# Kernel tuning notes

Measured on AMD Instinct MI355X. Metric: run time of the kernel, lower is better.

Reference implementation:

```python
import jax, jax.numpy as jnp
import numpy as np

N_NODES = 50000
N_EDGES = 800000
IN_FEATS = 256
HIDDEN = 256
NUM_CLASSES = 64


def setup_inputs() -> dict:
    key = jax.random.key(0)
    k1, k2, k3, k4 = jax.random.split(key, 4)
    features = jax.random.normal(k1, (N_NODES, IN_FEATS), dtype=jnp.float32)
    edge_index = jax.random.randint(k2, (2, N_EDGES), 0, N_NODES, dtype=jnp.int32)
    W1 = jax.random.normal(k3, (IN_FEATS, HIDDEN), dtype=jnp.float32) * (1.0 / np.sqrt(IN_FEATS))
    b1 = jnp.zeros((HIDDEN,), dtype=jnp.float32)
    W2 = jax.random.normal(k4, (HIDDEN, NUM_CLASSES), dtype=jnp.float32) * (1.0 / np.sqrt(HIDDEN))
    b2 = jnp.zeros((NUM_CLASSES,), dtype=jnp.float32)
    return {"features": features, "edge_index": edge_index, "W1": W1, "b1": b1, "W2": W2, "b2": b2}


def reference(features, edge_index, W1, b1, W2, b2):
    # Two-layer GCN: h = A_hat @ relu(A_hat @ X W1 + b1) W2 + b2
    # A_hat uses symmetric degree normalization 1/sqrt(d_src * d_dst)
    N = features.shape[0]
    src, dst = edge_index[0], edge_index[1]
    ones = jnp.ones((src.shape[0],), dtype=features.dtype)
    deg_out = jax.ops.segment_sum(ones, src, num_segments=N)  # out-degree per node
    deg_in = jax.ops.segment_sum(ones, dst, num_segments=N)   # in-degree per node
    inv_sqrt_out = jax.lax.rsqrt(jnp.maximum(deg_out, 1.0))
    inv_sqrt_in = jax.lax.rsqrt(jnp.maximum(deg_in, 1.0))
    edge_norm = (inv_sqrt_out[src] * inv_sqrt_in[dst])[:, None]  # [E,1]

    def gcn_layer(x, W, b):
        h = x @ W                      # transform first (reduces message width)
        msg = h[src] * edge_norm       # [E, out]
        agg = jax.ops.segment_sum(msg, dst, num_segments=N)
        return agg + b

    h = jax.nn.relu(gcn_layer(features, W1, b1))
    return gcn_layer(h, W2, b2)
```

## Files before the change

### kernel.cpp

```cpp
#include <hip/hip_runtime.h>

#define NN 50000
#define MPAD 50048
#define NE 800000
#define SCAN_BLOCKS 49

typedef short short8 __attribute__((ext_vector_type(8)));
typedef float f32x4 __attribute__((ext_vector_type(4)));

__device__ __forceinline__ unsigned short f2bf(float x) {
    unsigned u = __builtin_bit_cast(unsigned, x);
    u += 0x7FFFu + ((u >> 16) & 1u);
    return (unsigned short)(u >> 16);
}
__device__ __forceinline__ float bf2f(unsigned short h) {
    unsigned u = ((unsigned)h) << 16;
    return __builtin_bit_cast(float, u);
}
__device__ __forceinline__ void gld16(const void* g, void* l) {
    __builtin_amdgcn_global_load_lds(
        (const __attribute__((address_space(1))) unsigned int*)g,
        (__attribute__((address_space(3))) unsigned int*)l, 16, 0, 0);
}


__global__ __launch_bounds__(256) void count_kernel(const int* __restrict__ src,
    const int* __restrict__ dst, int* __restrict__ cnt_out, int* __restrict__ cnt_in, int E)
{
    int e = blockIdx.x * 256 + threadIdx.x;
    if (e < E) {
        atomicAdd(&cnt_out[src[e]], 1);
        atomicAdd(&cnt_in[dst[e]], 1);
    }
}

__global__ __launch_bounds__(256) void inv_kernel(const int* __restrict__ cnt_out,
    const int* __restrict__ cnt_in, float* __restrict__ inv_out, float* __restrict__ inv_in, int n)
{
    int i = blockIdx.x * 256 + threadIdx.x;
    if (i < n) {
        inv_out[i] = rsqrtf(fmaxf((float)cnt_out[i], 1.0f));
        inv_in[i]  = rsqrtf(fmaxf((float)cnt_in[i], 1.0f));
    }
}

__global__ __launch_bounds__(256) void scanA_kernel(const int* __restrict__ cnt,
    int* __restrict__ bsum)
{
    __shared__ int sm[256];
    int b = blockIdx.x, tid = threadIdx.x;
    int base = b * 1024 + tid * 4;
    int s = 0;
    #pragma unroll
    for (int i = 0; i < 4; ++i) {
        int idx = base + i;
        if (idx < NN) s += cnt[idx];
    }
    sm[tid] = s;
    __syncthreads();
    for (int off = 128; off > 0; off >>= 1) {
        if (tid < off) sm[tid] += sm[tid + off];
        __syncthreads();
    }
    if (tid == 0) bsum[b] = sm[0];
}

__global__ __launch_bounds__(64) void scanB_kernel(const int* __restrict__ bsum,
    int* __restrict__ bexcl)
{
    int tid = threadIdx.x;
    int orig = (tid < SCAN_BLOCKS) ? bsum[tid] : 0;
    int v = orig;
    #pragma unroll
    for (int off = 1; off < 64; off <<= 1) {
        int u = __shfl_up(v, off, 64);
        if (tid >= off) v += u;
    }
    if (tid < SCAN_BLOCKS) bexcl[tid] = v - orig;
}

__global__ __launch_bounds__(256) void scanC_kernel(const int* __restrict__ cnt,
    const int* __restrict__ bexcl, int* __restrict__ rs)
{
    __shared__ int wsum[4];
    int b = blockIdx.x, tid = threadIdx.x;
    int lane = tid & 63, wv = tid >> 6;
    int base = b * 1024 + tid * 4;
    int v[4]; int s = 0;
    #pragma unroll
    for (int i = 0; i < 4; ++i) {
        int idx = base + i;
        v[i] = (idx < NN) ? cnt[idx] : 0;
        s += v[i];
    }
    int inc = s;
    #pragma unroll
    for (int off = 1; off < 64; off <<= 1) {
        int u = __shfl_up(inc, off, 64);
        if (lane >= off) inc += u;
    }
    if (lane == 63) wsum[wv] = inc;
    __syncthreads();
    int wo = 0;
    for (int i = 0; i < wv; ++i) wo += wsum[i];
    int run = wo + (inc - s) + bexcl[b];
    #pragma unroll
    for (int i = 0; i < 4; ++i) {
        int idx = base + i;
        if (idx < NN) { rs[idx] = run; run += v[i]; }
    }
}

__global__ __launch_bounds__(256) void fill_kernel(const int* __restrict__ src,
    const int* __restrict__ dst, int* __restrict__ rs, int* __restrict__ csr_src, int E)
{
    int e = blockIdx.x * 256 + threadIdx.x;
    if (e < E) {
        int slot = atomicAdd(&rs[dst[e]], 1);
        csr_src[slot] = src[e];
    }
}

__global__ __launch_bounds__(256) void splitX_kernel(const float* __restrict__ X,
    unsigned short* __restrict__ Xh, unsigned short* __restrict__ Xl)
{
    int i = blockIdx.x * 256 + threadIdx.x;
    if (i >= NN * 32) return;
    int r = i >> 5, c = i & 31;
    const float* src = X + (size_t)r * 256 + c * 8;
    float4 a0 = *(const float4*)src;
    float4 a1 = *(const float4*)(src + 4);
    float xs[8] = {a0.x, a0.y, a0.z, a0.w, a1.x, a1.y, a1.z, a1.w};
    short8 hv, lv;
    #pragma unroll
    for (int t = 0; t < 8; ++t) {
        unsigned short h = f2bf(xs[t]);
        hv[t] = (short)h;
        lv[t] = (short)f2bf(xs[t] - bf2f(h));
    }
    size_t off = (size_t)r * 256 + (c >> 3) * 64 + (((c & 7) ^ (r & 7)) * 8);
    *(short8*)&Xh[off] = hv;
    *(short8*)&Xl[off] = lv;
}

__global__ __launch_bounds__(256) void splitW_kernel(const float* __restrict__ W,
    unsigned short* __restrict__ BT, int N)
{
    int i = blockIdx.x * 256 + threadIdx.x;
    if (i >= N * 32) return;
    int col = i >> 5, kc = i & 31;
    short8 hv, lv;
    #pragma unroll
    for (int j = 0; j < 8; ++j) {
        float x = W[(size_t)(kc * 8 + j) * N + col];
        unsigned short h = f2bf(x);
        hv[j] = (short)h;
        lv[j] = (short)f2bf(x - bf2f(h));
    }
    size_t base = (size_t)col * 512;
    size_t o = (kc >> 3) * 64 + (((kc & 7) ^ (col & 7)) * 8);
    *(short8*)&BT[base + o] = hv;
    *(short8*)&BT[base + 256 + o] = lv;
}

template<int BN, bool SWZ_OUT>
__global__ __launch_bounds__(256) void gemm_sp_kernel(
    const unsigned short* __restrict__ Ah, const unsigned short* __restrict__ Al,
    const unsigned short* __restrict__ BT, const float* __restrict__ inv_out,
    unsigned short* __restrict__ C, int M, int Ntot)
{
    constexpr int WN = BN / 2;
    constexpr int NF = WN / 16;
    constexpr int BI = BN / 32;
    __shared__ unsigned short As[128 * 64];
    __shared__ unsigned short Bs[BN * 64];
    const int tid = threadIdx.x;
    const int w = tid >> 6, lane = tid & 63;
    const int wm = w >> 1, wn = w & 1;
    const int r = lane & 15, kg = lane >> 4;
    const int rowbase = blockIdx.x * 128;
    const int colbase = blockIdx.y * BN;

    f32x4 acc[4][NF] = {};

    for (int t = 0; t < 12; ++t) {
        const int ph = t >> 2;
        const int kb = t & 3;
        const unsigned short* Asrc = (ph == 1) ? Al : Ah;
        const int bsel = (ph == 2) ? 256 : 0;
        #pragma unroll
        for (int i = 0; i < 4; ++i) {
            int ct = (w * 4 + i) * 64 + lane;
            int row = ct >> 3, c = ct & 7;
            gld16(Asrc + (size_t)(rowbase + row) * 256 + kb * 64 + c * 8,
                  (unsigned short*)As + (size_t)ct * 8);
        }
        #pragma unroll
        for (int i = 0; i < BI; ++i) {
            int ct = (w * BI + i) * 64 + lane;
            int col = ct >> 3, c = ct & 7;
            gld16(BT + (size_t)(colbase + col) * 512 + bsel + kb * 64 + c * 8,
                  (unsigned short*)Bs + (size_t)ct * 8);
        }
        __syncthreads();
        #pragma unroll
        for (int ks = 0; ks < 2; ++ks) {
            short8 af[4];
            #pragma unroll
            for (int mf = 0; mf < 4; ++mf) {
                int row = wm * 64 + mf * 16 + r;
                af[mf] = *(const short8*)&As[row * 64 + (((ks * 4 + kg) ^ (row & 7)) * 8)];
            }
            #pragma unroll
            for (int nf = 0; nf < NF; ++nf) {
                int col = wn * WN + nf * 16 + r;
                short8 bf = *(const short8*)&Bs[col * 64 + (((ks * 4 + kg) ^ (col & 7)) * 8)];
                #pragma unroll
                for (int mf = 0; mf < 4; ++mf)
                    acc[mf][nf] = __builtin_amdgcn_mfma_f32_16x16x32_bf16(af[mf], bf, acc[mf][nf], 0, 0, 0);
            }
        }
        __syncthreads();
    }

    #pragma unroll
    for (int mf = 0; mf < 4; ++mf) {
        #pragma unroll
        for (int reg = 0; reg < 4; ++reg) {
            int orow = rowbase + wm * 64 + mf * 16 + kg * 4 + reg;
            if (orow >= M) continue;
            float sc = inv_out[orow];
            #pragma unroll
            for (int nf = 0; nf < NF; ++nf) {
                int ocol = colbase + wn * WN + nf * 16 + r;
                unsigned short v = f2bf(acc[mf][nf][reg] * sc);
                if (SWZ_OUT) {
                    size_t idx = (size_t)orow * 256 + (ocol >> 6) * 64
                               + ((((ocol >> 3) & 7) ^ (orow & 7)) * 8) + (ocol & 7);
                    C[idx] = v;
                } else {
                    C[(size_t)orow * Ntot + ocol] = v;
                }
            }
        }
    }
}

__global__ __launch_bounds__(256) void gather256_kernel(const unsigned short* __restrict__ t1s,
    const int* __restrict__ csr_src, const int* __restrict__ rs,
    const float* __restrict__ inv_in, const float* __restrict__ b1,
    unsigned short* __restrict__ Ah2, unsigned short* __restrict__ Al2)
{
    int n = (int)((blockIdx.x * 256 + threadIdx.x) >> 6);
    int lane = threadIdx.x & 63;
    if (n >= NN) return;
    int begin = (n == 0) ? 0 : rs[n - 1];
    int end = rs[n];
    int c = lane >> 1, h = lane & 1;
    int cc = c & 7;
    int sub = (c >> 3) * 64 + h * 4;
    float a0 = 0.f, a1 = 0.f, a2 = 0.f, a3 = 0.f;
    #pragma unroll 2
    for (int j = begin; j < end; ++j) {
        int s = csr_src[j];
        ushort4 v = *(const ushort4*)&t1s[(size_t)s * 256 + sub + ((cc ^ (s & 7)) * 8)];
        a0 += bf2f(v.x); a1 += bf2f(v.y); a2 += bf2f(v.z); a3 += bf2f(v.w);
    }
    float win = inv_in[n];
    int k0 = c * 8 + h * 4;
    float4 bb = *(const float4*)&b1[k0];
    float x0 = fmaxf(fmaf(a0, win, bb.x), 0.f);
    float x1 = fmaxf(fmaf(a1, win, bb.y), 0.f);
    float x2 = fmaxf(fmaf(a2, win, bb.z), 0.f);
    float x3 = fmaxf(fmaf(a3, win, bb.w), 0.f);
    unsigned short h0 = f2bf(x0), h1 = f2bf(x1), h2 = f2bf(x2), h3 = f2bf(x3);
    ushort4 hv = {h0, h1, h2, h3};
    ushort4 lv = {f2bf(x0 - bf2f(h0)), f2bf(x1 - bf2f(h1)),
                  f2bf(x2 - bf2f(h2)), f2bf(x3 - bf2f(h3))};
    size_t off = (size_t)n * 256 + sub + ((cc ^ (n & 7)) * 8);
    *(ushort4*)&Ah2[off] = hv;
    *(ushort4*)&Al2[off] = lv;
}

__global__ __launch_bounds__(256) void gather64_kernel(const unsigned short* __restrict__ t2,
    const int* __restrict__ csr_src, const int* __restrict__ rs,
    const float* __restrict__ inv_in, const float* __restrict__ b2,
    float* __restrict__ out)
{
    int n = (int)((blockIdx.x * 256 + threadIdx.x) >> 6);
    int lane = threadIdx.x & 63;
    if (n >= NN) return;
    int begin = (n == 0) ? 0 : rs[n - 1];
    int end = rs[n];
    float acc = 0.f;
    #pragma unroll 2
    for (int j = begin; j < end; ++j) {
        int s = csr_src[j];
        acc += bf2f(t2[(size_t)s * 64 + lane]);
    }
    out[(size_t)n * 64 + lane] = fmaf(acc, inv_in[n], b2[lane]);
}

extern "C" void kernel_launch(void* const* d_in, const int* in_sizes, int n_in,
                              void* d_out, int out_size, void* d_ws, size_t ws_size,
                              hipStream_t stream)
{
    const float* features = (const float*)d_in[0];
    const int*   edge_index = (const int*)d_in[1];
    const float* W1 = (const float*)d_in[2];
    const float* b1 = (const float*)d_in[3];
    const float* W2 = (const float*)d_in[4];
    const float* b2 = (const float*)d_in[5];
    float* out = (float*)d_out;
    const int* src = edge_index;
    const int* dst = edge_index + NE;

    char* p = (char*)d_ws;
    int* cnt_out = (int*)p;            p += (size_t)NN * 4;
    int* cnt_in  = (int*)p;            p += (size_t)NN * 4;
    float* inv_out = (float*)p;        p += (size_t)NN * 4;
    float* inv_in  = (float*)p;        p += (size_t)NN * 4;
    int* rs      = (int*)p;            p += (size_t)NN * 4;
    int* csr_src = (int*)p;            p += (size_t)NE * 4;
    int* bsum    = (int*)p;            p += 64 * 4;
    int* bexcl   = (int*)p;            p += 64 * 4;
    unsigned short* W1T = (unsigned short*)p;  p += (size_t)256 * 512 * 2;
    unsigned short* W2T = (unsigned short*)p;  p += (size_t)64 * 512 * 2;
    unsigned short* Xh  = (unsigned short*)p;  p += (size_t)MPAD * 256 * 2;
    unsigned short* Xl  = (unsigned short*)p;  p += (size_t)MPAD * 256 * 2;
    unsigned short* t1s = (unsigned short*)p;  p += (size_t)NN * 256 * 2;
    unsigned short* Ah2 = (unsigned short*)p;  p += (size_t)MPAD * 256 * 2;
    unsigned short* Al2 = (unsigned short*)p;  p += (size_t)MPAD * 256 * 2;
    unsigned short* t2  = (unsigned short*)p;  p += (size_t)NN * 64 * 2;

    hipMemsetAsync(cnt_out, 0, 2 * (size_t)NN * sizeof(int), stream);

    count_kernel<<<(NE + 255) / 256, 256, 0, stream>>>(src, dst, cnt_out, cnt_in, NE);
    inv_kernel<<<(NN + 255) / 256, 256, 0, stream>>>(cnt_out, cnt_in, inv_out, inv_in, NN);
    scanA_kernel<<<SCAN_BLOCKS, 256, 0, stream>>>(cnt_in, bsum);
    scanB_kernel<<<1, 64, 0, stream>>>(bsum, bexcl);
    scanC_kernel<<<SCAN_BLOCKS, 256, 0, stream>>>(cnt_in, bexcl, rs);
    fill_kernel<<<(NE + 255) / 256, 256, 0, stream>>>(src, dst, rs, csr_src, NE);

    splitX_kernel<<<(NN * 32 + 255) / 256, 256, 0, stream>>>(features, Xh, Xl);
    splitW_kernel<<<(256 * 32 + 255) / 256, 256, 0, stream>>>(W1, W1T, 256);
    splitW_kernel<<<(64 * 32 + 255) / 256, 256, 0, stream>>>(W2, W2T, 64);

    gemm_sp_kernel<128, true><<<dim3(MPAD / 128, 2), 256, 0, stream>>>(
        Xh, Xl, W1T, inv_out, t1s, NN, 256);

    gather256_kernel<<<(NN * 64 + 255) / 256, 256, 0, stream>>>(
        t1s, csr_src, rs, inv_in, b1, Ah2, Al2);

    gemm_sp_kernel<64, false><<<dim3(MPAD / 128, 1), 256, 0, stream>>>(
        Ah2, Al2, W2T, inv_out, t2, NN, 64);

    gather64_kernel<<<(NN * 64 + 255) / 256, 256, 0, stream>>>(
        t2, csr_src, rs, inv_in, b2, out);
}
```

Measured before the change: 343.0 us.

## Fuse split-bf16 GEMM phases into one K loop and unroll gather loops by four

The split-precision GEMM previously made three separate passes over K (hi*hi, lo*hi, hi*lo), reloading A and B tiles each time. It now loads the hi and lo tiles of A and B together and issues all three MFMAs per fragment in a single pass, which cuts the number of global-to-LDS loads and barriers. The cost is twice the LDS footprint and more registers per thread, which may lower occupancy. The two gather kernels are also manually unrolled by four so more independent neighbor loads are in flight.

```diff
diff --git a/kernel.cpp b/kernel.cpp
--- a/kernel.cpp
+++ b/kernel.cpp
@@ -172,8 +172,10 @@
     constexpr int WN = BN / 2;
     constexpr int NF = WN / 16;
     constexpr int BI = BN / 32;
-    __shared__ unsigned short As[128 * 64];
-    __shared__ unsigned short Bs[BN * 64];
+    __shared__ unsigned short Ash[128 * 64];
+    __shared__ unsigned short Asl[128 * 64];
+    __shared__ unsigned short Bsh[BN * 64];
+    __shared__ unsigned short Bsl[BN * 64];
     const int tid = threadIdx.x;
     const int w = tid >> 6, lane = tid & 63;
     const int wm = w >> 1, wn = w & 1;
@@ -183,41 +185,46 @@
 
     f32x4 acc[4][NF] = {};
 
-    for (int t = 0; t < 12; ++t) {
-        const int ph = t >> 2;
-        const int kb = t & 3;
-        const unsigned short* Asrc = (ph == 1) ? Al : Ah;
-        const int bsel = (ph == 2) ? 256 : 0;
+    for (int kb = 0; kb < 4; ++kb) {
         #pragma unroll
         for (int i = 0; i < 4; ++i) {
             int ct = (w * 4 + i) * 64 + lane;
             int row = ct >> 3, c = ct & 7;
-            gld16(Asrc + (size_t)(rowbase + row) * 256 + kb * 64 + c * 8,
-                  (unsigned short*)As + (size_t)ct * 8);
+            size_t goff = (size_t)(rowbase + row) * 256 + kb * 64 + c * 8;
+            gld16(Ah + goff, (unsigned short*)Ash + (size_t)ct * 8);
+            gld16(Al + goff, (unsigned short*)Asl + (size_t)ct * 8);
         }
         #pragma unroll
         for (int i = 0; i < BI; ++i) {
             int ct = (w * BI + i) * 64 + lane;
             int col = ct >> 3, c = ct & 7;
-            gld16(BT + (size_t)(colbase + col) * 512 + bsel + kb * 64 + c * 8,
-                  (unsigned short*)Bs + (size_t)ct * 8);
+            size_t goff = (size_t)(colbase + col) * 512 + kb * 64 + c * 8;
+            gld16(BT + goff, (unsigned short*)Bsh + (size_t)ct * 8);
+            gld16(BT + goff + 256, (unsigned short*)Bsl + (size_t)ct * 8);
         }
         __syncthreads();
         #pragma unroll
         for (int ks = 0; ks < 2; ++ks) {
-            short8 af[4];
+            short8 ahf[4], alf[4];
             #pragma unroll
             for (int mf = 0; mf < 4; ++mf) {
                 int row = wm * 64 + mf * 16 + r;
-                af[mf] = *(const short8*)&As[row * 64 + (((ks * 4 + kg) ^ (row & 7)) * 8)];
+                int lo = row * 64 + (((ks * 4 + kg) ^ (row & 7)) * 8);
+                ahf[mf] = *(const short8*)&Ash[lo];
+                alf[mf] = *(const short8*)&Asl[lo];
             }
             #pragma unroll
             for (int nf = 0; nf < NF; ++nf) {
                 int col = wn * WN + nf * 16 + r;
-                short8 bf = *(const short8*)&Bs[col * 64 + (((ks * 4 + kg) ^ (col & 7)) * 8)];
+                int lo = col * 64 + (((ks * 4 + kg) ^ (col & 7)) * 8);
+                short8 bh = *(const short8*)&Bsh[lo];
+                short8 bl = *(const short8*)&Bsl[lo];
                 #pragma unroll
-                for (int mf = 0; mf < 4; ++mf)
-                    acc[mf][nf] = __builtin_amdgcn_mfma_f32_16x16x32_bf16(af[mf], bf, acc[mf][nf], 0, 0, 0);
+                for (int mf = 0; mf < 4; ++mf) {
+                    acc[mf][nf] = __builtin_amdgcn_mfma_f32_16x16x32_bf16(ahf[mf], bh, acc[mf][nf], 0, 0, 0);
+                    acc[mf][nf] = __builtin_amdgcn_mfma_f32_16x16x32_bf16(alf[mf], bh, acc[mf][nf], 0, 0, 0);
+                    acc[mf][nf] = __builtin_amdgcn_mfma_f32_16x16x32_bf16(ahf[mf], bl, acc[mf][nf], 0, 0, 0);
+                }
             }
         }
         __syncthreads();
@@ -260,8 +267,19 @@
     int cc = c & 7;
     int sub = (c >> 3) * 64 + h * 4;
     float a0 = 0.f, a1 = 0.f, a2 = 0.f, a3 = 0.f;
-    #pragma unroll 2
-    for (int j = begin; j < end; ++j) {
+    int j = begin;
+    for (; j + 4 <= end; j += 4) {
+        int s0 = csr_src[j], s1 = csr_src[j + 1], s2 = csr_src[j + 2], s3 = csr_src[j + 3];
+        ushort4 v0 = *(const ushort4*)&t1s[(size_t)s0 * 256 + sub + ((cc ^ (s0 & 7)) * 8)];
+        ushort4 v1 = *(const ushort4*)&t1s[(size_t)s1 * 256 + sub + ((cc ^ (s1 & 7)) * 8)];
+        ushort4 v2 = *(const ushort4*)&t1s[(size_t)s2 * 256 + sub + ((cc ^ (s2 & 7)) * 8)];
+        ushort4 v3 = *(const ushort4*)&t1s[(size_t)s3 * 256 + sub + ((cc ^ (s3 & 7)) * 8)];
+        a0 += bf2f(v0.x); a1 += bf2f(v0.y); a2 += bf2f(v0.z); a3 += bf2f(v0.w);
+        a0 += bf2f(v1.x); a1 += bf2f(v1.y); a2 += bf2f(v1.z); a3 += bf2f(v1.w);
+        a0 += bf2f(v2.x); a1 += bf2f(v2.y); a2 += bf2f(v2.z); a3 += bf2f(v2.w);
+        a0 += bf2f(v3.x); a1 += bf2f(v3.y); a2 += bf2f(v3.z); a3 += bf2f(v3.w);
+    }
+    for (; j < end; ++j) {
         int s = csr_src[j];
         ushort4 v = *(const ushort4*)&t1s[(size_t)s * 256 + sub + ((cc ^ (s & 7)) * 8)];
         a0 += bf2f(v.x); a1 += bf2f(v.y); a2 += bf2f(v.z); a3 += bf2f(v.w);
@@ -293,8 +311,16 @@
     int begin = (n == 0) ? 0 : rs[n - 1];
     int end = rs[n];
     float acc = 0.f;
-    #pragma unroll 2
-    for (int j = begin; j < end; ++j) {
+    int j = begin;
+    for (; j + 4 <= end; j += 4) {
+        int s0 = csr_src[j], s1 = csr_src[j + 1], s2 = csr_src[j + 2], s3 = csr_src[j + 3];
+        float v0 = bf2f(t2[(size_t)s0 * 64 + lane]);
+        float v1 = bf2f(t2[(size_t)s1 * 64 + lane]);
+        float v2 = bf2f(t2[(size_t)s2 * 64 + lane]);
+        float v3 = bf2f(t2[(size_t)s3 * 64 + lane]);
+        acc += v0; acc += v1; acc += v2; acc += v3;
+    }
+    for (; j < end; ++j) {
         int s = csr_src[j];
         acc += bf2f(t2[(size_t)s * 64 + lane]);
     }
```

New measurement: 320.6 us. -6.5%, faster.
